# Optimization experiments

Hardware: AMD Instinct MI355X
Metric: run time of the kernel (lower is better)

Reference implementation:

```python
import jax, jax.numpy as jnp
import numpy as np

LOG_2PI = float(np.log(2.0 * np.pi))
EPS = 1e-6


def setup_inputs() -> dict:
    key = jax.random.key(0)
    ks = jax.random.split(key, 7)
    T, D, S = 24, 262144, 12
    recog_J = jax.random.uniform(ks[0], (T, D), minval=0.5, maxval=1.5)  # positive precisions
    recog_h = jax.random.normal(ks[1], (T, D)) * 0.1
    loc = jax.random.normal(ks[2], (D,)) * 0.1
    Tau = 1.0 + 0.1 * jax.random.normal(ks[3], (D,))
    Lambda = 1.0 + 0.1 * jax.random.normal(ks[4], (S, D))
    A = 0.9 + 0.05 * jax.random.normal(ks[5], (S, D))
    b = 0.1 * jax.random.normal(ks[6], (S, D))
    return {"recog_J": recog_J, "recog_h": recog_h, "loc": loc, "Tau": Tau,
            "Lambda": Lambda, "A": A, "b": b}


def _tile(x, T):
    # concat([x, x[:-1]]) as in the module, truncated to the T-1 transitions
    return jnp.concatenate([x, x[:-1]], axis=0)[: T - 1]


def reference(recog_J, recog_h, loc, Tau, Lambda, A, b):
    T, D = recog_J.shape
    tau = Tau ** 2 + EPS                      # init precision (D,)
    tau_mu = tau * loc
    lam = Lambda ** 2 + EPS                   # transition precision (12, D)
    # natural params of pairwise potential -lam/2 (x' - A x - b)^2 (constants dropped)
    Jaa = _tile(A ** 2 * lam, T)              # (T-1, D) precision on x_t
    Jab = _tile(A * lam, T)                   # cross term (+Jab x_t x_{t+1})
    Jbb = _tile(lam, T)                       # precision on x_{t+1}
    ha = _tile(-(A * lam * b), T)             # linear on x_t
    hb = _tile(lam * b, T)                    # linear on x_{t+1}

    # ---- forward information filter over the chain (scalar Kalman per dim) ----
    fJ0 = tau + recog_J[0]
    fh0 = tau_mu + recog_h[0]

    def fstep(carry, inp):
        fJ, fh, logZ = carry
        jaa, jab, jbb, ha_t, hb_t, rJ, rh = inp
        denom = fJ + jaa
        hc = fh + ha_t
        logZ = logZ + 0.5 * (LOG_2PI - jnp.log(denom)) + hc ** 2 / (2.0 * denom)
        fJn = jbb - jab ** 2 / denom + rJ
        fhn = hb_t + jab * hc / denom + rh
        return (fJn, fhn, logZ), (fJn, fhn)

    (fJT, fhT, logZ_acc), (fJs, fhs) = jax.lax.scan(
        fstep, (fJ0, fh0, jnp.zeros_like(fJ0)),
        (Jaa, Jab, Jbb, ha, hb, recog_J[1:], recog_h[1:]))
    fJ_all = jnp.concatenate([fJ0[None], fJs], axis=0)  # (T, D) filtered precision
    fh_all = jnp.concatenate([fh0[None], fhs], axis=0)  # (T, D) filtered h
    q_logZ = jnp.sum(logZ_acc + 0.5 * (LOG_2PI - jnp.log(fJT)) + fhT ** 2 / (2.0 * fJT))

    # ---- backward (RTS) smoother: E[x_t], E[x_t^2] ----
    ExT = fhT / fJT
    VarT = 1.0 / fJT

    def bstep(carry, inp):
        Exn, Varn = carry
        fJ, fh, jaa, jab, ha_t = inp
        denom = fJ + jaa
        g = jab / denom
        Ex = (fh + ha_t + jab * Exn) / denom
        Var = 1.0 / denom + g ** 2 * Varn
        return (Ex, Var), (Ex, Var)

    _, (Ex_rest, Var_rest) = jax.lax.scan(
        bstep, (ExT, VarT), (fJ_all[:-1], fh_all[:-1], Jaa, Jab, ha), reverse=True)
    Ex = jnp.concatenate([Ex_rest, ExT[None]], axis=0)
    Exx = jnp.concatenate([Var_rest, VarT[None]], axis=0) + Ex ** 2

    # ---- backward posterior sampling (temp = 1) ----
    eps = jax.random.normal(jax.random.key(0), (T, D), dtype=recog_J.dtype)
    zT = ExT + eps[-1] / jnp.sqrt(fJT)

    def sstep(zn, inp):
        fJ, fh, jaa, jab, ha_t, e = inp
        denom = fJ + jaa
        z = (fh + ha_t + jab * zn) / denom + e / jnp.sqrt(denom)
        return z, z

    _, z_rest = jax.lax.scan(sstep, zT,
                             (fJ_all[:-1], fh_all[:-1], Jaa, Jab, ha, eps[:-1]),
                             reverse=True)
    z = jnp.concatenate([z_rest, zT[None]], axis=0)  # (T, D)

    # ---- prior log-normalizer (constants dropped from natural potentials) ----
    init_norm = 0.5 * (LOG_2PI * D + jnp.sum(tau * loc ** 2) - jnp.sum(jnp.log(tau)))
    trans_norm = 0.5 * (LOG_2PI * D * (T - 1)
                        + jnp.sum(_tile(lam * b ** 2, T))
                        - jnp.sum(_tile(jnp.log(lam), T)))
    p_logZ = init_norm + trans_norm

    # KL(q||p) = <recog_potentials, E_q[stats]> - q_logZ + p_logZ
    kl = jnp.sum(-0.5 * recog_J * Exx + recog_h * Ex) - q_logZ + p_logZ
    return z, kl, Ex, Exx
```

## Files before the change

kernel.cpp:

```cpp
#include <hip/hip_runtime.h>
#include <stdint.h>

#define D_DIM 262144
#define T_DIM 24
#define S_DIM 12
#define BLK 256
#define NBLK (D_DIM / BLK)
#define LDS_T 19

static constexpr float EPSF = 1e-6f;

__device__ __forceinline__ void tf_round(unsigned& x0, unsigned& x1, int r) {
  x0 += x1;
  x1 = (x1 << r) | (x1 >> (32 - r));
  x1 ^= x0;
}

__device__ __forceinline__ void threefry00(unsigned c0, unsigned c1,
                                           unsigned& o0, unsigned& o1) {
  const unsigned ks0 = 0u, ks1 = 0u, ks2 = 0x1BD11BDAu;
  unsigned x0 = c0 + ks0, x1 = c1 + ks1;
  tf_round(x0, x1, 13); tf_round(x0, x1, 15); tf_round(x0, x1, 26); tf_round(x0, x1, 6);
  x0 += ks1; x1 += ks2 + 1u;
  tf_round(x0, x1, 17); tf_round(x0, x1, 29); tf_round(x0, x1, 16); tf_round(x0, x1, 24);
  x0 += ks2; x1 += ks0 + 2u;
  tf_round(x0, x1, 13); tf_round(x0, x1, 15); tf_round(x0, x1, 26); tf_round(x0, x1, 6);
  x0 += ks0; x1 += ks1 + 3u;
  tf_round(x0, x1, 17); tf_round(x0, x1, 29); tf_round(x0, x1, 16); tf_round(x0, x1, 24);
  x0 += ks1; x1 += ks2 + 4u;
  tf_round(x0, x1, 13); tf_round(x0, x1, 15); tf_round(x0, x1, 26); tf_round(x0, x1, 6);
  x0 += ks2; x1 += ks0 + 5u;
  o0 = x0; o1 = x1;
}

__device__ __forceinline__ float bits_to_normal(unsigned bits) {
  const float lo = -0.99999994f;
  const float hi = 1.0f;
  unsigned fb = (bits >> 9) | 0x3f800000u;
  float f = __uint_as_float(fb) - 1.0f;
  float u = f * (hi - lo) + lo;
  u = fmaxf(lo, u);
  float w = -__logf(fmaf(-u, u, 1.0f));
  float p;
  if (w < 5.0f) {
    w = w - 2.5f;
    p = 2.81022636e-08f;
    p = fmaf(p, w, 3.43273939e-07f);
    p = fmaf(p, w, -3.5233877e-06f);
    p = fmaf(p, w, -4.39150654e-06f);
    p = fmaf(p, w, 0.00021858087f);
    p = fmaf(p, w, -0.00125372503f);
    p = fmaf(p, w, -0.00417768164f);
    p = fmaf(p, w, 0.246640727f);
    p = fmaf(p, w, 1.50140941f);
  } else {
    w = sqrtf(w) - 3.0f;
    p = -0.000200214257f;
    p = fmaf(p, w, 0.000100950558f);
    p = fmaf(p, w, 0.00134934322f);
    p = fmaf(p, w, -0.00367342844f);
    p = fmaf(p, w, 0.00573950773f);
    p = fmaf(p, w, -0.0076224613f);
    p = fmaf(p, w, 0.00943887047f);
    p = fmaf(p, w, 1.00167406f);
    p = fmaf(p, w, 2.83297682f);
  }
  return 1.41421356237309515f * (p * u);
}

__global__ __launch_bounds__(256) void pgm_lds_kernel(
    const float* __restrict__ recog_J, const float* __restrict__ recog_h,
    const float* __restrict__ loc_p, const float* __restrict__ Tau_p,
    const float* __restrict__ Lambda_p, const float* __restrict__ A_p,
    const float* __restrict__ b_p,
    float* __restrict__ z_out,
    float* __restrict__ Ex_out, float* __restrict__ Exx_out,
    float* __restrict__ kl_partials) {
  __shared__ float s_rJ[LDS_T * BLK];
  __shared__ float s_rh[LDS_T * BLK];
  __shared__ float s_kl[BLK / 64];
  const int tid = threadIdx.x;
  const int d = blockIdx.x * BLK + tid;

#define RJ(t) (((t) < LDS_T) ? s_rJ[(t) * BLK + tid]                           \
                             : recog_J[(size_t)(t) * D_DIM + d])
#define RH(t) (((t) < LDS_T) ? s_rh[(t) * BLK + tid]                           \
                             : recog_h[(size_t)(t) * D_DIM + d])

#pragma unroll
  for (int t = 0; t < LDS_T; ++t) {
    __builtin_amdgcn_global_load_lds(
        (const __attribute__((address_space(1))) uint32_t*)(uintptr_t)(recog_J + (size_t)t * D_DIM + d),
        (__attribute__((address_space(3))) uint32_t*)(uintptr_t)(s_rJ + t * BLK + tid),
        4, 0, 0);
    __builtin_amdgcn_global_load_lds(
        (const __attribute__((address_space(1))) uint32_t*)(uintptr_t)(recog_h + (size_t)t * D_DIM + d),
        (__attribute__((address_space(3))) uint32_t*)(uintptr_t)(s_rh + t * BLK + tid),
        4, 0, 0);
  }

  float lam[S_DIM], Aa[S_DIM], hb[S_DIM];
  float kld = 0.0f;
#pragma unroll
  for (int s = 0; s < S_DIM; ++s) {
    float L = Lambda_p[s * D_DIM + d];
    float a = A_p[s * D_DIM + d];
    float bb = b_p[s * D_DIM + d];
    float l = L * L + EPSF;
    lam[s] = l;
    Aa[s] = a;
    hb[s] = l * bb;
    float wgt = (s < 11) ? 1.0f : 0.5f;
    kld += wgt * (hb[s] * bb - __logf(l));
  }
  float tau, tau_mu;
  {
    float Tv = Tau_p[d];
    float lv = loc_p[d];
    tau = Tv * Tv + EPSF;
    tau_mu = tau * lv;
    kld += 0.5f * (tau * lv * lv - __logf(tau));
  }

  __syncthreads();

  float fJ[T_DIM], fh[T_DIM];
  fJ[0] = tau + RJ(0);
  fh[0] = tau_mu + RH(0);
#pragma unroll
  for (int t = 0; t < T_DIM - 1; ++t) {
    const int s = (t < 12) ? t : t - 12;
    float l = lam[s], a = Aa[s];
    float jab = a * l;
    float jaa = a * jab;
    float ha = -a * hb[s];
    float denom = fJ[t] + jaa;
    float inv = __builtin_amdgcn_rcpf(denom);
    float hc = fh[t] + ha;
    kld += 0.5f * __logf(denom) - 0.5f * hc * hc * inv;
    fJ[t + 1] = l - jab * jab * inv + RJ(t + 1);
    fh[t + 1] = hb[s] + jab * hc * inv + RH(t + 1);
  }
  const float fJT = fJ[T_DIM - 1];
  const float fhT = fh[T_DIM - 1];
  const float invT = __builtin_amdgcn_rcpf(fJT);
  kld += 0.5f * __logf(fJT) - 0.5f * fhT * fhT * invT;

  float eps_st[S_DIM];
  float ExT = fhT * invT;
  float VarT = invT;
  float eps23;
  {
    unsigned o0, o1;
    threefry00((unsigned)(11 * D_DIM + d), (unsigned)(23 * D_DIM + d), o0, o1);
    eps_st[11] = bits_to_normal(o0);
    eps23 = bits_to_normal(o1);
  }
  float zT = ExT + eps23 * sqrtf(invT);
  float ExxT = VarT + ExT * ExT;
  kld += -0.5f * RJ(T_DIM - 1) * ExxT + RH(T_DIM - 1) * ExT;
  z_out[(T_DIM - 1) * D_DIM + d] = zT;
  Ex_out[(T_DIM - 1) * D_DIM + d] = ExT;
  Exx_out[(T_DIM - 1) * D_DIM + d] = ExxT;

  float Exn = ExT, Varn = VarT, zn = zT;
#pragma unroll
  for (int t = T_DIM - 2; t >= 0; --t) {
    const int s = (t < 12) ? t : t - 12;
    float l = lam[s], a = Aa[s];
    float jab = a * l;
    float jaa = a * jab;
    float ha = -a * hb[s];
    float denom = fJ[t] + jaa;
    float inv = __builtin_amdgcn_rcpf(denom);
    float hc = fh[t] + ha;

    float e;
    if (t >= 12) {
      unsigned o0, o1;
      threefry00((unsigned)((t - 12) * D_DIM + d), (unsigned)(t * D_DIM + d), o0, o1);
      eps_st[t - 12] = bits_to_normal(o0);
      e = bits_to_normal(o1);
    } else {
      e = eps_st[t];
    }

    float g = jab * inv;
    float Ex = (hc + jab * Exn) * inv;
    float Var = inv + g * g * Varn;
    float zt = (hc + jab * zn) * inv + e * sqrtf(inv);
    float Exx = Var + Ex * Ex;
    kld += -0.5f * RJ(t) * Exx + RH(t) * Ex;

    z_out[t * D_DIM + d] = zt;
    Ex_out[t * D_DIM + d] = Ex;
    Exx_out[t * D_DIM + d] = Exx;

    Exn = Ex; Varn = Var; zn = zt;
  }

#pragma unroll
  for (int off = 32; off > 0; off >>= 1)
    kld += __shfl_down(kld, off, 64);
  if ((tid & 63) == 0)
    s_kl[tid >> 6] = kld;
  __syncthreads();
  if (tid == 0)
    kl_partials[blockIdx.x] = s_kl[0] + s_kl[1] + s_kl[2] + s_kl[3];
}

__global__ __launch_bounds__(256) void kl_reduce_kernel(
    const float* __restrict__ kl_partials, float* __restrict__ kl_out) {
  __shared__ float s_kl[BLK / 64];
  float v = 0.0f;
#pragma unroll
  for (int i = 0; i < NBLK / BLK; ++i)
    v += kl_partials[i * BLK + threadIdx.x];
#pragma unroll
  for (int off = 32; off > 0; off >>= 1)
    v += __shfl_down(v, off, 64);
  if ((threadIdx.x & 63) == 0)
    s_kl[threadIdx.x >> 6] = v;
  __syncthreads();
  if (threadIdx.x == 0)
    kl_out[0] = s_kl[0] + s_kl[1] + s_kl[2] + s_kl[3];
}

extern "C" void kernel_launch(void* const* d_in, const int* in_sizes, int n_in,
                              void* d_out, int out_size, void* d_ws, size_t ws_size,
                              hipStream_t stream) {
  const float* recog_J = (const float*)d_in[0];
  const float* recog_h = (const float*)d_in[1];
  const float* loc_p   = (const float*)d_in[2];
  const float* Tau_p   = (const float*)d_in[3];
  const float* Lambda_p = (const float*)d_in[4];
  const float* A_p     = (const float*)d_in[5];
  const float* b_p     = (const float*)d_in[6];

  float* out = (float*)d_out;
  float* z_out  = out;
  float* kl_out = out + (size_t)T_DIM * D_DIM;
  float* Ex_out = kl_out + 1;
  float* Exx_out = Ex_out + (size_t)T_DIM * D_DIM;
  float* kl_partials = (float*)d_ws;

  pgm_lds_kernel<<<dim3(NBLK), dim3(BLK), 0, stream>>>(
      recog_J, recog_h, loc_p, Tau_p, Lambda_p, A_p, b_p,
      z_out, Ex_out, Exx_out, kl_partials);
  kl_reduce_kernel<<<dim3(1), dim3(BLK), 0, stream>>>(kl_partials, kl_out);
}
```

Before: 46.66 us.

## Precompute Gaussian noise in separate kernel and batch logs into products

Moves the threefry plus inverse-erf noise generation into a separate kernel that writes eps into the Exx output buffer. The main kernel then reads each eps back just before overwriting that slot. It also cuts transcendental work by replacing per-step logs with logs of running products (lam, tau, denominators). This takes heavy ALU work off the latency-bound recurrence kernel, but adds an extra 24xD write and read of global memory plus a kernel launch, and the product of logs risks overflow or precision loss.

```diff
diff --git a/kernel.cpp b/kernel.cpp
--- a/kernel.cpp
+++ b/kernel.cpp
@@ -6,6 +6,7 @@
 #define S_DIM 12
 #define BLK 256
 #define NBLK (D_DIM / BLK)
+#define HALF_N (S_DIM * D_DIM)
 #define LDS_T 19
 
 static constexpr float EPSF = 1e-6f;
@@ -68,6 +69,14 @@
   return 1.41421356237309515f * (p * u);
 }
 
+__global__ __launch_bounds__(256) void eps_kernel(float* __restrict__ eps) {
+  const int j = blockIdx.x * blockDim.x + threadIdx.x;
+  unsigned o0, o1;
+  threefry00((unsigned)j, (unsigned)(j + HALF_N), o0, o1);
+  eps[j] = bits_to_normal(o0);
+  eps[j + HALF_N] = bits_to_normal(o1);
+}
+
 __global__ __launch_bounds__(256) void pgm_lds_kernel(
     const float* __restrict__ recog_J, const float* __restrict__ recog_h,
     const float* __restrict__ loc_p, const float* __restrict__ Tau_p,
@@ -101,6 +110,7 @@
 
   float lam[S_DIM], Aa[S_DIM], hb[S_DIM];
   float kld = 0.0f;
+  float prodA = 1.0f;
 #pragma unroll
   for (int s = 0; s < S_DIM; ++s) {
     float L = Lambda_p[s * D_DIM + d];
@@ -111,7 +121,8 @@
     Aa[s] = a;
     hb[s] = l * bb;
     float wgt = (s < 11) ? 1.0f : 0.5f;
-    kld += wgt * (hb[s] * bb - __logf(l));
+    kld += wgt * (hb[s] * bb);
+    if (s < 11) prodA *= l;
   }
   float tau, tau_mu;
   {
@@ -119,14 +130,16 @@
     float lv = loc_p[d];
     tau = Tv * Tv + EPSF;
     tau_mu = tau * lv;
-    kld += 0.5f * (tau * lv * lv - __logf(tau));
-  }
+    kld += 0.5f * (tau * lv * lv);
+  }
+  kld -= __logf(prodA) + 0.5f * __logf(lam[11] * tau);
 
   __syncthreads();
 
   float fJ[T_DIM], fh[T_DIM];
   fJ[0] = tau + RJ(0);
   fh[0] = tau_mu + RH(0);
+  float prodD = 1.0f;
 #pragma unroll
   for (int t = 0; t < T_DIM - 1; ++t) {
     const int s = (t < 12) ? t : t - 12;
@@ -137,25 +150,21 @@
     float denom = fJ[t] + jaa;
     float inv = __builtin_amdgcn_rcpf(denom);
     float hc = fh[t] + ha;
-    kld += 0.5f * __logf(denom) - 0.5f * hc * hc * inv;
+    prodD *= denom;
+    kld += -0.5f * hc * hc * inv;
+    if (t == 11) { kld += 0.5f * __logf(prodD); prodD = 1.0f; }
     fJ[t + 1] = l - jab * jab * inv + RJ(t + 1);
     fh[t + 1] = hb[s] + jab * hc * inv + RH(t + 1);
   }
   const float fJT = fJ[T_DIM - 1];
   const float fhT = fh[T_DIM - 1];
   const float invT = __builtin_amdgcn_rcpf(fJT);
-  kld += 0.5f * __logf(fJT) - 0.5f * fhT * fhT * invT;
-
-  float eps_st[S_DIM];
+  prodD *= fJT;
+  kld += 0.5f * __logf(prodD) - 0.5f * fhT * fhT * invT;
+
   float ExT = fhT * invT;
   float VarT = invT;
-  float eps23;
-  {
-    unsigned o0, o1;
-    threefry00((unsigned)(11 * D_DIM + d), (unsigned)(23 * D_DIM + d), o0, o1);
-    eps_st[11] = bits_to_normal(o0);
-    eps23 = bits_to_normal(o1);
-  }
+  float eps23 = Exx_out[(T_DIM - 1) * D_DIM + d];
   float zT = ExT + eps23 * sqrtf(invT);
   float ExxT = VarT + ExT * ExT;
   kld += -0.5f * RJ(T_DIM - 1) * ExxT + RH(T_DIM - 1) * ExT;
@@ -175,15 +184,7 @@
     float inv = __builtin_amdgcn_rcpf(denom);
     float hc = fh[t] + ha;
 
-    float e;
-    if (t >= 12) {
-      unsigned o0, o1;
-      threefry00((unsigned)((t - 12) * D_DIM + d), (unsigned)(t * D_DIM + d), o0, o1);
-      eps_st[t - 12] = bits_to_normal(o0);
-      e = bits_to_normal(o1);
-    } else {
-      e = eps_st[t];
-    }
+    float e = Exx_out[t * D_DIM + d];
 
     float g = jab * inv;
     float Ex = (hc + jab * Exn) * inv;
@@ -244,6 +245,7 @@
   float* Exx_out = Ex_out + (size_t)T_DIM * D_DIM;
   float* kl_partials = (float*)d_ws;
 
+  eps_kernel<<<dim3(HALF_N / BLK), dim3(BLK), 0, stream>>>(Exx_out);
   pgm_lds_kernel<<<dim3(NBLK), dim3(BLK), 0, stream>>>(
       recog_J, recog_h, loc_p, Tau_p, Lambda_p, A_p, b_p,
       z_out, Ex_out, Exx_out, kl_partials);
```

New measurement: 57.24 us. 22.7% more time.
